# Kernel tuning notes

Hardware: AMD Instinct MI355X
Metric: run time of the kernel (lower is better)

## Reference

```python
import jax, jax.numpy as jnp
import numpy as np
from functools import partial

VOCAB = 32000
N_LAYER = 2
D_MODEL = 1024
D_INNER = 2048   # expand * d_model
D_STATE = 16
D_CONV = 4
DT_RANK = 64     # ceil(d_model/16)
SEQ_LEN = 2048   # == D_INNER (required by the repo's conv quirk)
BATCH = 1
EPS = 1e-6


def rmsnorm(x, scale):
    return x * jax.lax.rsqrt(jnp.mean(x * x, axis=-1, keepdims=True) + EPS) * scale


def setup_inputs() -> dict:
    key = jax.random.key(0)
    ks = jax.random.split(key, 16)
    s = 0.02
    L = N_LAYER
    inp = {
        "input_ids": jax.random.randint(ks[0], (BATCH, SEQ_LEN), 0, VOCAB, dtype=jnp.int32),
        "embed": jax.random.normal(ks[1], (VOCAB, D_MODEL), jnp.float32) * s,
        "norm_scale": jnp.ones((L, D_MODEL), jnp.float32),
        "in_proj_w": jax.random.normal(ks[2], (L, D_MODEL, 2 * D_INNER), jnp.float32) * s,
        "in_proj_b": jnp.zeros((L, 2 * D_INNER), jnp.float32),
        "conv_w": jax.random.normal(ks[3], (L, D_CONV, 1, SEQ_LEN), jnp.float32) * s,
        "conv_b": jnp.zeros((L, SEQ_LEN), jnp.float32),
        "x_proj_w": jax.random.normal(ks[4], (L, D_MODEL, DT_RANK + 2 * D_STATE), jnp.float32) * s,
        "dt_proj_w": jax.random.normal(ks[5], (L, DT_RANK, D_INNER), jnp.float32) * s,
        "dt_proj_b": jnp.zeros((L, D_INNER), jnp.float32),
        "out_proj_w": jax.random.normal(ks[6], (L, D_INNER, D_MODEL), jnp.float32) * s,
        "out_proj_b": jnp.zeros((L, D_MODEL), jnp.float32),
        "A_log": jnp.tile(jnp.log(jnp.arange(1, D_STATE + 1, dtype=jnp.float32)), (L, D_INNER, 1)),
        "D_param": jnp.ones((L, D_INNER), jnp.float32),
        "norm_f_scale": jnp.ones((D_MODEL,), jnp.float32),
        "lm_head_w": jax.random.normal(ks[7], (D_MODEL, VOCAB), jnp.float32) * s,
    }
    return inp


def selective_scan(u, delta, A, B, C, D):
    # u, delta: (b,l,d)   A: (d,n)   B,C: (b,l,n)   D: (d,)
    deltaA = jnp.exp(jnp.einsum('bld,dn->bldn', delta, A))            # (b,l,d,n)
    deltaB_u = delta[..., None] * B[:, :, None, :] * u[..., None]      # (b,l,d,n)

    def step(x, inps):
        dA, dBu, c = inps            # (b,d,n),(b,d,n),(b,n)
        x = dA * x + dBu
        y = jnp.einsum('bdn,bn->bd', x, c)
        return x, y

    x0 = jnp.zeros((u.shape[0], u.shape[2], A.shape[1]), u.dtype)
    _, ys = jax.lax.scan(step, x0, (jnp.moveaxis(deltaA, 1, 0),
                                    jnp.moveaxis(deltaB_u, 1, 0),
                                    jnp.moveaxis(C, 1, 0)))
    return jnp.moveaxis(ys, 0, 1) + u * D                              # (b,l,d)


def depthwise_conv(x, w, b):
    # Faithful to repo: Conv(features=SEQ_LEN, groups=D_INNER) on (b, d_inner, l).
    # With SEQ_LEN == D_INNER this is a depthwise conv over the d_inner axis.
    # x: (b, d_inner, l) as (N, W, C);  w: (d_conv, 1, SEQ_LEN)
    y = jax.lax.conv_general_dilated(x, w, window_strides=(1,), padding='SAME',
                                     dimension_numbers=('NWC', 'WIO', 'NWC'),
                                     feature_group_count=SEQ_LEN)
    return y + b


def mamba_block(h, norm_scale, in_w, in_b, conv_w, conv_b, x_proj_w,
                dt_w, dt_b, out_w, out_b, A_log, Dp):
    u = rmsnorm(h, norm_scale)
    A = -jnp.exp(A_log)
    x_and_res = u @ in_w + in_b
    x, res = jnp.split(x_and_res, 2, axis=-1)
    xt = jnp.transpose(x, (0, 2, 1))                 # (b, d_inner, l)
    xt = depthwise_conv(xt, conv_w, conv_b)[:, :, :u.shape[1]]
    x = jax.nn.silu(jnp.transpose(xt, (0, 2, 1)))     # (b, l, d_inner)
    x_dbl = u @ x_proj_w
    delta, B, C = jnp.split(x_dbl, [DT_RANK, DT_RANK + D_STATE], axis=-1)
    delta = jax.nn.softplus(delta @ dt_w + dt_b)
    y = selective_scan(x, delta, A, B, C, Dp)
    y = y * jax.nn.silu(res)
    return y @ out_w + out_b + h


def reference(input_ids, embed, norm_scale, in_proj_w, in_proj_b, conv_w, conv_b,
              x_proj_w, dt_proj_w, dt_proj_b, out_proj_w, out_proj_b, A_log,
              D_param, norm_f_scale, lm_head_w):
    h = embed[input_ids]                              # (b,l,d_model)
    for i in range(N_LAYER):
        h = mamba_block(h, norm_scale[i], in_proj_w[i], in_proj_b[i], conv_w[i],
                        conv_b[i], x_proj_w[i], dt_proj_w[i], dt_proj_b[i],
                        out_proj_w[i], out_proj_b[i], A_log[i], D_param[i])
    h = rmsnorm(h, norm_f_scale)
    return h @ lm_head_w                              # (b,l,vocab)
```

## Files before the change

### kernel.cpp

```cpp
#include <hip/hip_runtime.h>
#include <hip/hip_bf16.h>

#define SEQ 2048
#define DM  1024
#define DI  2048
#define DST 16
#define DTR 64
#define NVOC 32000
#define NVOCP 32768
#define NC  64
#define LC  32

typedef __bf16 bf16x8 __attribute__((ext_vector_type(8)));
typedef float  f32x4  __attribute__((ext_vector_type(4)));

__device__ __forceinline__ float siluf(float x) { return x / (1.f + expf(-x)); }
__device__ __forceinline__ float softplusf(float x) {
    return fmaxf(x, 0.f) + log1pf(expf(-fabsf(x)));
}
__device__ __forceinline__ unsigned short f2bf(float f) {
    union { __hip_bfloat16 h; unsigned short u; } c;
    c.h = __float2bfloat16(f);
    return c.u;
}

__global__ void embed_gather(const int* __restrict__ ids, const float* __restrict__ embed,
                             float* __restrict__ h) {
    int l = blockIdx.x;
    int row = ids[l];
    const float4* src = (const float4*)(embed + (size_t)row * DM);
    float4* dst = (float4*)(h + (size_t)l * DM);
    dst[threadIdx.x] = src[threadIdx.x];
}

__global__ void rmsnorm_kernel(const float* __restrict__ x, const float* __restrict__ w,
                               float* __restrict__ o, unsigned short* __restrict__ ob) {
    int l = blockIdx.x;
    int t = threadIdx.x;
    float4 v = ((const float4*)(x + (size_t)l * DM))[t];
    float ss = v.x*v.x + v.y*v.y + v.z*v.z + v.w*v.w;
    #pragma unroll
    for (int m = 32; m; m >>= 1) ss += __shfl_xor(ss, m);
    __shared__ float red[4];
    if ((t & 63) == 0) red[t >> 6] = ss;
    __syncthreads();
    float tot = red[0] + red[1] + red[2] + red[3];
    float sc = rsqrtf(tot * (1.f / DM) + 1e-6f);
    float4 wv = ((const float4*)w)[t];
    float4 ov;
    ov.x = v.x * sc * wv.x;
    ov.y = v.y * sc * wv.y;
    ov.z = v.z * sc * wv.z;
    ov.w = v.w * sc * wv.w;
    if (ob) {
        uint2 pk;
        pk.x = (unsigned)f2bf(ov.x) | ((unsigned)f2bf(ov.y) << 16);
        pk.y = (unsigned)f2bf(ov.z) | ((unsigned)f2bf(ov.w) << 16);
        ((uint2*)(ob + (size_t)l * DM))[t] = pk;
    } else {
        ((float4*)(o + (size_t)l * DM))[t] = ov;
    }
}

__global__ void transpose_all(const float* __restrict__ in_w, const float* __restrict__ xp_w,
                              const float* __restrict__ out_w, const float* __restrict__ dt_w,
                              const float* __restrict__ lm_w,
                              unsigned short* __restrict__ in_wT, unsigned short* __restrict__ out_wT,
                              unsigned short* __restrict__ dt_wT, unsigned short* __restrict__ lm_wT) {
    int b = blockIdx.x;
    const float* W; unsigned short* WT; int K, N, Np, loc;
    if      (b < 1024)  { W = in_w;                        WT = in_wT;                                             K=1024; N=4096;  Np=4096;  loc = b; }
    else if (b < 1056)  { W = xp_w;                        WT = in_wT + (size_t)4096 * 1024;                       K=1024; N=96;    Np=128;   loc = b - 1024; }
    else if (b < 2080)  { W = in_w + (size_t)1024 * 4096;  WT = in_wT + (size_t)4224 * 1024;                       K=1024; N=4096;  Np=4096;  loc = b - 1056; }
    else if (b < 2112)  { W = xp_w + (size_t)1024 * 96;    WT = in_wT + (size_t)4224 * 1024 + (size_t)4096 * 1024; K=1024; N=96;    Np=128;   loc = b - 2080; }
    else if (b < 2624)  { W = out_w;                       WT = out_wT;                                            K=2048; N=1024;  Np=1024;  loc = b - 2112; }
    else if (b < 3136)  { W = out_w + (size_t)2048 * 1024; WT = out_wT + (size_t)1024 * 2048;                      K=2048; N=1024;  Np=1024;  loc = b - 2624; }
    else if (b < 3168)  { W = dt_w;                        WT = dt_wT;                                             K=64;   N=2048;  Np=2048;  loc = b - 3136; }
    else if (b < 3200)  { W = dt_w + (size_t)64 * 2048;    WT = dt_wT + (size_t)2048 * 64;                         K=64;   N=2048;  Np=2048;  loc = b - 3168; }
    else                { if (!lm_wT) return; W = lm_w;    WT = lm_wT;                                             K=1024; N=32000; Np=32768; loc = b - 3200; }
    int tiles_x = Np >> 6;
    int n0 = (loc % tiles_x) * 64, k0 = (loc / tiles_x) * 64;
    __shared__ float tile[64][65];
    int tx = threadIdx.x;
    int ty = threadIdx.y;
    #pragma unroll
    for (int i = 0; i < 8; i++) {
        int r = ty + i * 8;
        int n1 = n0 + tx, n2 = n0 + tx + 32;
        tile[tx][r]      = (n1 < N) ? W[(size_t)(k0 + r) * N + n1] : 0.f;
        tile[tx + 32][r] = (n2 < N) ? W[(size_t)(k0 + r) * N + n2] : 0.f;
    }
    __syncthreads();
    int t = ty * 32 + tx;
    int nrow = t >> 5;
    int u = t & 31;
    #pragma unroll
    for (int pass = 0; pass < 8; pass++) {
        int n = pass * 8 + nrow;
        unsigned v = (unsigned)f2bf(tile[n][2 * u]) | ((unsigned)f2bf(tile[n][2 * u + 1]) << 16);
        *(unsigned*)&WT[(size_t)(n0 + n) * K + k0 + 2 * u] = v;
    }
}

template<int ACT>
__global__ __launch_bounds__(256) void gemm_f32(const float* __restrict__ A, int lda,
                                                const float* __restrict__ B,
                                                const float* __restrict__ bias,
                                                const float* __restrict__ add,
                                                float* __restrict__ C,
                                                int M, int N, int K) {
    __shared__ float As[16][68];
    __shared__ float Bs[16][64];
    int tx = threadIdx.x, ty = threadIdx.y;
    int t = ty * 16 + tx;
    int m0 = blockIdx.y * 64, n0 = blockIdx.x * 64;
    float acc[4][4] = {};
    for (int k0 = 0; k0 < K; k0 += 16) {
        #pragma unroll
        for (int i = 0; i < 4; i++) {
            int idx = t + i * 256;
            int mm = idx >> 4, kk = idx & 15;
            As[kk][mm] = A[(size_t)(m0 + mm) * lda + k0 + kk];
            int nn = idx & 63, k2 = idx >> 6;
            Bs[k2][nn] = B[(size_t)(k0 + k2) * N + n0 + nn];
        }
        __syncthreads();
        #pragma unroll
        for (int kk = 0; kk < 16; kk++) {
            float4 a = *(const float4*)&As[kk][ty * 4];
            float4 b = *(const float4*)&Bs[kk][tx * 4];
            acc[0][0] += a.x*b.x; acc[0][1] += a.x*b.y; acc[0][2] += a.x*b.z; acc[0][3] += a.x*b.w;
            acc[1][0] += a.y*b.x; acc[1][1] += a.y*b.y; acc[1][2] += a.y*b.z; acc[1][3] += a.y*b.w;
            acc[2][0] += a.z*b.x; acc[2][1] += a.z*b.y; acc[2][2] += a.z*b.z; acc[2][3] += a.z*b.w;
            acc[3][0] += a.w*b.x; acc[3][1] += a.w*b.y; acc[3][2] += a.w*b.z; acc[3][3] += a.w*b.w;
        }
        __syncthreads();
    }
    #pragma unroll
    for (int i = 0; i < 4; i++) {
        int row = m0 + ty * 4 + i;
        float4 r;
        float* pr = &r.x;
        #pragma unroll
        for (int j = 0; j < 4; j++) {
            int col = n0 + tx * 4 + j;
            float v = acc[i][j];
            if (bias) v += bias[col];
            if (add)  v += add[(size_t)row * N + col];
            if (ACT == 1) v = softplusf(v);
            pr[j] = v;
        }
        *(float4*)&C[(size_t)row * N + n0 + tx * 4] = r;
    }
}

template<int BIAS, int ADD, int ACT, int XP>
__global__ __launch_bounds__(256) void gemm_bf16(const unsigned short* __restrict__ A, int lda,
                                                 const unsigned short* __restrict__ BT,
                                                 const float* __restrict__ bias,
                                                 const float* __restrict__ add,
                                                 float* __restrict__ C,
                                                 float* __restrict__ xp_out,
                                                 unsigned short* __restrict__ aux,
                                                 int M, int N, int K) {
    __shared__ unsigned short As[128 * 32];
    __shared__ unsigned short Bs[128 * 32];
    int t = threadIdx.x;
    int w = t >> 6, l = t & 63;
    int wm = w >> 1, wn = w & 1;
    int m0 = blockIdx.x * 128;
    int n0 = blockIdx.y * 128;
    int lr = l & 15, lk = (l >> 4) * 8;
    int sr = t >> 2, sc = (t & 3) * 8;
    f32x4 acc[4][4] = {};
    for (int k0 = 0; k0 < K; k0 += 32) {
        const unsigned short* ga = A  + (size_t)(m0 + sr) * lda + k0 + sc;
        const unsigned short* gb = BT + (size_t)(n0 + sr) * K + k0 + sc;
        unsigned short* la = As + w * 512;
        unsigned short* lb = Bs + w * 512;
        __builtin_amdgcn_global_load_lds((const __attribute__((address_space(1))) void*)ga,
            (__attribute__((address_space(3))) void*)la, 16, 0, 0);
        __builtin_amdgcn_global_load_lds((const __attribute__((address_space(1))) void*)(ga + (size_t)64 * lda),
            (__attribute__((address_space(3))) void*)(la + 2048), 16, 0, 0);
        __builtin_amdgcn_global_load_lds((const __attribute__((address_space(1))) void*)gb,
            (__attribute__((address_space(3))) void*)(lb), 16, 0, 0);
        __builtin_amdgcn_global_load_lds((const __attribute__((address_space(1))) void*)(gb + (size_t)64 * K),
            (__attribute__((address_space(3))) void*)(lb + 2048), 16, 0, 0);
        __syncthreads();
        bf16x8 af[4], bfr[4];
        #pragma unroll
        for (int i = 0; i < 4; i++) {
            af[i]  = *reinterpret_cast<const bf16x8*>(&As[(wm * 64 + i * 16 + lr) * 32 + lk]);
            bfr[i] = *reinterpret_cast<const bf16x8*>(&Bs[(wn * 64 + i * 16 + lr) * 32 + lk]);
        }
        #pragma unroll
        for (int i = 0; i < 4; i++)
            #pragma unroll
            for (int j = 0; j < 4; j++)
                acc[i][j] = __builtin_amdgcn_mfma_f32_16x16x32_bf16(af[i], bfr[j], acc[i][j], 0, 0, 0);
        __syncthreads();
    }
    int cr = (l >> 4) * 4;
    if (XP && n0 >= 4096) {
        #pragma unroll
        for (int i = 0; i < 4; i++) {
            #pragma unroll
            for (int j = 0; j < 4; j++) {
                int c2 = (n0 - 4096) + wn * 64 + j * 16 + lr;
                #pragma unroll
                for (int rr = 0; rr < 4; rr++) {
                    int row = m0 + wm * 64 + i * 16 + cr + rr;
                    float v = acc[i][j][rr];
                    xp_out[(size_t)row * 128 + c2] = v;
                    if (c2 < 64) aux[(size_t)row * 64 + c2] = f2bf(v);
                }
            }
        }
    } else {
        int ldc = XP ? 4096 : N;
        #pragma unroll
        for (int i = 0; i < 4; i++) {
            #pragma unroll
            for (int j = 0; j < 4; j++) {
                int col = n0 + wn * 64 + j * 16 + lr;
                float bv = BIAS ? bias[col] : 0.f;
                #pragma unroll
                for (int rr = 0; rr < 4; rr++) {
                    int row = m0 + wm * 64 + i * 16 + cr + rr;
                    float v = acc[i][j][rr] + bv;
                    if (ADD) v += add[(size_t)row * ldc + col];
                    if (ACT == 1) v = softplusf(v);
                    C[(size_t)row * ldc + col] = v;
                }
            }
        }
    }
}

__global__ __launch_bounds__(1024, 4) void gemm_lm(
        const unsigned short* __restrict__ A,
        const unsigned short* __restrict__ BT,
        float* __restrict__ C, int M, int N, int K) {
    extern __shared__ unsigned short lds[];
    const int t = threadIdx.x;
    const int w = t >> 6, l = t & 63;
    const int wr = w >> 2, wc = w & 3;
    int bxx = blockIdx.x, byy = blockIdx.y;
    if (gridDim.x == 8 && (gridDim.y & 7) == 0) {
        int lin = blockIdx.y * 8 + blockIdx.x;
        int xcd = lin & 7, i = lin >> 3;
        bxx = i & 7;
        byy = xcd * (gridDim.y >> 3) + (i >> 3);
    }
    const int m0 = bxx * 256, n0 = byy * 256;
    const int lr = l & 15;
    const int rowA = wr * 64 + lr;
    const int rowB = wc * 64 + lr;
    const int colR = (((l >> 4) ^ (lr & 3)) * 8);
    const int srow = t >> 2;
    const int scol = (((t & 3) ^ (srow & 3)) * 8);
    const int NT = K >> 5;
    f32x4 acc[4][4] = {};
    bf16x8 af[4], bf[4];

    const unsigned short* gA = A  + (size_t)(m0 + srow) * K + scol;
    const unsigned short* gB = BT + (size_t)(n0 + srow) * K + scol;

    #pragma unroll
    for (int pp = 0; pp < 2; pp++) {
        if (pp < NT) {
            unsigned short* Ld = lds + pp * 16384;
            __builtin_amdgcn_global_load_lds(
                (const __attribute__((address_space(1))) void*)(gA + pp * 32),
                (__attribute__((address_space(3))) void*)(Ld + w * 512), 16, 0, 0);
            __builtin_amdgcn_global_load_lds(
                (const __attribute__((address_space(1))) void*)(gB + pp * 32),
                (__attribute__((address_space(3))) void*)(Ld + 8192 + w * 512), 16, 0, 0);
        }
    }

    for (int kt = 0; kt < NT; kt++) {
        if (kt >= NT - 2) { asm volatile("s_waitcnt vmcnt(0)" ::: "memory"); }
        else              { asm volatile("s_waitcnt vmcnt(2)" ::: "memory"); }
        __builtin_amdgcn_sched_barrier(0);
        __builtin_amdgcn_s_barrier();
        __builtin_amdgcn_sched_barrier(0);
        const unsigned short* Ab = lds + (kt % 3) * 16384;
        const unsigned short* Bb = Ab + 8192;
        #pragma unroll
        for (int i = 0; i < 4; i++)
            af[i] = *reinterpret_cast<const bf16x8*>(&Ab[(rowA + i * 16) * 32 + colR]);
        #pragma unroll
        for (int j = 0; j < 4; j++)
            bf[j] = *reinterpret_cast<const bf16x8*>(&Bb[(rowB + j * 16) * 32 + colR]);
        if (kt + 2 < NT) {
            unsigned short* Ld = lds + ((kt + 2) % 3) * 16384;
            __builtin_amdgcn_global_load_lds(
                (const __attribute__((address_space(1))) void*)(gA + (kt + 2) * 32),
                (__attribute__((address_space(3))) void*)(Ld + w * 512), 16, 0, 0);
            __builtin_amdgcn_global_load_lds(
                (const __attribute__((address_space(1))) void*)(gB + (kt + 2) * 32),
                (__attribute__((address_space(3))) void*)(Ld + 8192 + w * 512), 16, 0, 0);
        }
        __builtin_amdgcn_s_setprio(1);
        #pragma unroll
        for (int i = 0; i < 4; i++)
            #pragma unroll
            for (int j = 0; j < 4; j++)
                acc[i][j] = __builtin_amdgcn_mfma_f32_16x16x32_bf16(af[i], bf[j], acc[i][j], 0, 0, 0);
        __builtin_amdgcn_s_setprio(0);
    }

    float* cf = (float*)lds;
    const int cr = (l >> 4) * 4;
    for (int r = 0; r < 4; r++) {
        __syncthreads();
        if (wr == r) {
            #pragma unroll
            for (int i = 0; i < 4; i++)
                #pragma unroll
                for (int j = 0; j < 4; j++) {
                    int col = wc * 64 + j * 16 + lr;
                    #pragma unroll
                    for (int rr = 0; rr < 4; rr++)
                        cf[(i * 16 + cr + rr) * 260 + col] = acc[i][j][rr];
                }
        }
        __syncthreads();
        #pragma unroll
        for (int pass = 0; pass < 4; pass++) {
            int row = pass * 16 + (t >> 6);
            int f4 = t & 63;
            f32x4 v = *(const f32x4*)&cf[row * 260 + f4 * 4];
            int grow = m0 + r * 64 + row;
            int gcol = n0 + f4 * 4;
            if (gcol < N)
                __builtin_nontemporal_store(v, (f32x4*)&C[(size_t)grow * N + gcol]);
        }
    }
}

__global__ void xproj_kernel(const float* __restrict__ u, const float* __restrict__ xw,
                             float* __restrict__ xdbl) {
    int l0 = blockIdx.x * 4;
    int t = threadIdx.x;
    __shared__ float us[4][DM];
    for (int i = t; i < 4 * DM; i += 128) us[i >> 10][i & 1023] = u[(size_t)l0 * DM + i];
    __syncthreads();
    if (t < 96) {
        float a0 = 0.f, a1 = 0.f, a2 = 0.f, a3 = 0.f;
        for (int k = 0; k < DM; k++) {
            float wv = xw[(size_t)k * 96 + t];
            a0 += us[0][k] * wv; a1 += us[1][k] * wv;
            a2 += us[2][k] * wv; a3 += us[3][k] * wv;
        }
        xdbl[(size_t)(l0 + 0) * 128 + t] = a0;
        xdbl[(size_t)(l0 + 1) * 128 + t] = a1;
        xdbl[(size_t)(l0 + 2) * 128 + t] = a2;
        xdbl[(size_t)(l0 + 3) * 128 + t] = a3;
    }
}

__global__ __launch_bounds__(256) void scan_p1(const float* __restrict__ xr,
        const float* __restrict__ delta, const float* __restrict__ xdbl,
        const float* __restrict__ cw, const float* __restrict__ cb,
        const float* __restrict__ A_log, float* __restrict__ P, float* __restrict__ S) {
    int c = blockIdx.x;
    int d = blockIdx.y * 256 + threadIdx.x;
    int l0 = c * LC;
    __shared__ float Bsh[LC][16];
    __shared__ float cwsh[4][LC];
    __shared__ float cbsh[LC];
    {
        int t = threadIdx.x;
        #pragma unroll
        for (int i = t; i < LC * 16; i += 256) {
            int ll = i >> 4, q = i & 15;
            Bsh[ll][q] = xdbl[(size_t)(l0 + ll) * 128 + 64 + q];
        }
        if (t < LC) {
            cbsh[t] = cb[l0 + t];
            #pragma unroll
            for (int k = 0; k < 4; k++) cwsh[k][t] = cw[k * SEQ + l0 + t];
        }
    }
    __syncthreads();
    float a[16];
    #pragma unroll
    for (int i = 0; i < 4; i++) {
        float4 al = ((const float4*)(A_log + (size_t)d * 16))[i];
        a[4*i+0] = -expf(al.x); a[4*i+1] = -expf(al.y);
        a[4*i+2] = -expf(al.z); a[4*i+3] = -expf(al.w);
    }
    float s[16] = {};
    float sumdv = 0.f;
    for (int ll = 0; ll < LC; ll++) {
        size_t lrow = (size_t)(l0 + ll);
        float dv = delta[lrow * DI + d];
        const float* xrow = xr + lrow * 4096;
        float accv = cbsh[ll];
        #pragma unroll
        for (int k = 0; k < 4; k++) {
            int cc = d + k - 1;
            if (cc >= 0 && cc < DI) accv += xrow[cc] * cwsh[k][ll];
        }
        float xv = siluf(accv);
        float du = dv * xv;
        sumdv += dv;
        #pragma unroll
        for (int n = 0; n < 16; n++)
            s[n] = expf(dv * a[n]) * s[n] + du * Bsh[ll][n];
    }
    size_t o = ((size_t)c * DI + d) * 16;
    #pragma unroll
    for (int i = 0; i < 4; i++) {
        float4 sv = make_float4(s[4*i], s[4*i+1], s[4*i+2], s[4*i+3]);
        float4 pv = make_float4(expf(a[4*i]*sumdv), expf(a[4*i+1]*sumdv),
                                expf(a[4*i+2]*sumdv), expf(a[4*i+3]*sumdv));
        ((float4*)(S + o))[i] = sv;
        ((float4*)(P + o))[i] = pv;
    }
}

__global__ void scan_p2(const float* __restrict__ P, const float* __restrict__ S,
                        float* __restrict__ X) {
    int t = blockIdx.x * 256 + threadIdx.x;
    float x = 0.f;
    #pragma unroll 16
    for (int c = 0; c < NC; c++) {
        X[(size_t)c * (DI*16) + t] = x;
        x = P[(size_t)c * (DI*16) + t] * x + S[(size_t)c * (DI*16) + t];
    }
}

__global__ __launch_bounds__(256) void scan_p3(const float* __restrict__ xr,
        const float* __restrict__ delta, const float* __restrict__ xdbl,
        const float* __restrict__ cw, const float* __restrict__ cb,
        const float* __restrict__ A_log, const float* __restrict__ Dp,
        const float* __restrict__ X,
        float* __restrict__ y, unsigned short* __restrict__ yb) {
    int c = blockIdx.x;
    int d = blockIdx.y * 256 + threadIdx.x;
    int l0 = c * LC;
    __shared__ float Bsh[LC][16], Csh[LC][16];
    __shared__ float cwsh[4][LC];
    __shared__ float cbsh[LC];
    {
        int t = threadIdx.x;
        #pragma unroll
        for (int i = t; i < LC * 16; i += 256) {
            int ll = i >> 4, q = i & 15;
            size_t row = (size_t)(l0 + ll) * 128;
            Bsh[ll][q] = xdbl[row + 64 + q];
            Csh[ll][q] = xdbl[row + 80 + q];
        }
        if (t < LC) {
            cbsh[t] = cb[l0 + t];
            #pragma unroll
            for (int k = 0; k < 4; k++) cwsh[k][t] = cw[k * SEQ + l0 + t];
        }
    }
    __syncthreads();
    float a[16];
    #pragma unroll
    for (int i = 0; i < 4; i++) {
        float4 al = ((const float4*)(A_log + (size_t)d * 16))[i];
        a[4*i+0] = -expf(al.x); a[4*i+1] = -expf(al.y);
        a[4*i+2] = -expf(al.z); a[4*i+3] = -expf(al.w);
    }
    float s[16];
    size_t o = ((size_t)c * DI + d) * 16;
    #pragma unroll
    for (int i = 0; i < 4; i++) {
        float4 xv4 = ((const float4*)(X + o))[i];
        s[4*i] = xv4.x; s[4*i+1] = xv4.y; s[4*i+2] = xv4.z; s[4*i+3] = xv4.w;
    }
    float Dv = Dp[d];
    for (int ll = 0; ll < LC; ll++) {
        size_t lrow = (size_t)(l0 + ll);
        float dv = delta[lrow * DI + d];
        const float* xrow = xr + lrow * 4096;
        float accv = cbsh[ll];
        #pragma unroll
        for (int k = 0; k < 4; k++) {
            int cc = d + k - 1;
            if (cc >= 0 && cc < DI) accv += xrow[cc] * cwsh[k][ll];
        }
        float xv = siluf(accv);
        float du = dv * xv;
        float yv = 0.f;
        #pragma unroll
        for (int n = 0; n < 16; n++) {
            s[n] = expf(dv * a[n]) * s[n] + du * Bsh[ll][n];
            yv += s[n] * Csh[ll][n];
        }
        float res = xrow[2048 + d];
        float val = (yv + xv * Dv) * siluf(res);
        if (yb) yb[lrow * DI + d] = f2bf(val);
        else    y[lrow * DI + d] = val;
    }
}

extern "C" void kernel_launch(void* const* d_in, const int* in_sizes, int n_in,
                              void* d_out, int out_size, void* d_ws, size_t ws_size,
                              hipStream_t stream) {
    const int*   ids        = (const int*)d_in[0];
    const float* embed      = (const float*)d_in[1];
    const float* norm_scale = (const float*)d_in[2];
    const float* in_w       = (const float*)d_in[3];
    const float* in_b       = (const float*)d_in[4];
    const float* conv_w     = (const float*)d_in[5];
    const float* conv_b     = (const float*)d_in[6];
    const float* x_proj_w   = (const float*)d_in[7];
    const float* dt_w       = (const float*)d_in[8];
    const float* dt_b       = (const float*)d_in[9];
    const float* out_w      = (const float*)d_in[10];
    const float* out_b      = (const float*)d_in[11];
    const float* A_log      = (const float*)d_in[12];
    const float* Dp         = (const float*)d_in[13];
    const float* norm_f     = (const float*)d_in[14];
    const float* lm_w       = (const float*)d_in[15];

    float* out = (float*)d_out;

    char* p = (char*)d_ws;
    float* h  = (float*)p;  p += (size_t)SEQ * DM * 4;
    float* hn = (float*)p;  p += (size_t)SEQ * DM * 4;
    size_t base = (size_t)p - (size_t)d_ws;
    const size_t SZ_UB    = (size_t)SEQ * DM * 2;
    const size_t SZ_YB    = (size_t)SEQ * DI * 2;
    const size_t SZ_HNB   = (size_t)SEQ * DM * 2;
    const size_t SZ_DB    = (size_t)SEQ * 64 * 2;
    const size_t SZ_INWT  = (size_t)2 * 4224 * DM * 2;
    const size_t SZ_OUTWT = (size_t)2 * DM * DI * 2;
    const size_t SZ_DTWT  = (size_t)2 * DI * 64 * 2;
    const size_t SZ_LMWT  = (size_t)NVOCP * DM * 2;
    size_t need_mid  = base + SZ_UB + SZ_YB + SZ_HNB + SZ_DB + SZ_INWT + SZ_OUTWT + SZ_DTWT;
    size_t need_full = need_mid + SZ_LMWT;
    bool mid  = ws_size >= need_mid;
    bool full = ws_size >= need_full;

    unsigned short *u_b = nullptr, *y_b = nullptr, *hn_b = nullptr, *dlt_b = nullptr;
    unsigned short *in_wT = nullptr, *out_wT = nullptr, *dt_wT = nullptr, *lm_wT = nullptr;
    if (mid) {
        u_b    = (unsigned short*)p; p += SZ_UB;
        y_b    = (unsigned short*)p; p += SZ_YB;
        hn_b   = (unsigned short*)p; p += SZ_HNB;
        dlt_b  = (unsigned short*)p; p += SZ_DB;
        in_wT  = (unsigned short*)p; p += SZ_INWT;
        out_wT = (unsigned short*)p; p += SZ_OUTWT;
        dt_wT  = (unsigned short*)p; p += SZ_DTWT;
        if (full) { lm_wT = (unsigned short*)p; p += SZ_LMWT; }
    }

    float* u     = out;
    float* xr    = u + (size_t)SEQ * DM;
    float* xdbl  = xr + (size_t)SEQ * 4096;
    float* delta = xdbl + (size_t)SEQ * 128;
    float* y     = delta + (size_t)SEQ * DI;
    float* Pbuf  = y + (size_t)SEQ * DI;
    float* Sbuf  = Pbuf + (size_t)NC * DI * 16;
    float* Xbuf  = Sbuf + (size_t)NC * DI * 16;

    if (mid) {
        int nblocks = full ? 11392 : 3200;
        transpose_all<<<nblocks, dim3(32, 8), 0, stream>>>(
            in_w, x_proj_w, out_w, dt_w, lm_w, in_wT, out_wT, dt_wT, lm_wT);
    }

    embed_gather<<<SEQ, 256, 0, stream>>>(ids, embed, h);

    for (int L = 0; L < 2; L++) {
        rmsnorm_kernel<<<SEQ, 256, 0, stream>>>(h, norm_scale + (size_t)L * DM, u, u_b);
        if (mid) {
            gemm_bf16<1, 0, 0, 1><<<dim3(SEQ / 128, 4224 / 128), 256, 0, stream>>>(
                u_b, DM, in_wT + (size_t)L * 4224 * DM, in_b + (size_t)L * 4096, nullptr, xr,
                xdbl, dlt_b, SEQ, 4224, DM);
            gemm_bf16<1, 0, 1, 0><<<dim3(SEQ / 128, DI / 128), 256, 0, stream>>>(
                dlt_b, 64, dt_wT + (size_t)L * DI * 64, dt_b + (size_t)L * DI, nullptr, delta,
                nullptr, nullptr, SEQ, DI, 64);
        } else {
            gemm_f32<0><<<dim3(4096 / 64, SEQ / 64), dim3(16, 16), 0, stream>>>(
                u, DM, in_w + (size_t)L * DM * 4096, in_b + (size_t)L * 4096, nullptr, xr,
                SEQ, 4096, DM);
            xproj_kernel<<<SEQ / 4, 128, 0, stream>>>(u, x_proj_w + (size_t)L * DM * 96, xdbl);
            gemm_f32<1><<<dim3(DI / 64, SEQ / 64), dim3(16, 16), 0, stream>>>(
                xdbl, 128, dt_w + (size_t)L * DTR * DI, dt_b + (size_t)L * DI, nullptr, delta,
                SEQ, DI, DTR);
        }
        scan_p1<<<dim3(NC, DI / 256), 256, 0, stream>>>(
            xr, delta, xdbl, conv_w + (size_t)L * 4 * SEQ, conv_b + (size_t)L * SEQ,
            A_log + (size_t)L * DI * DST, Pbuf, Sbuf);
        scan_p2<<<DI * 16 / 256, 256, 0, stream>>>(Pbuf, Sbuf, Xbuf);
        scan_p3<<<dim3(NC, DI / 256), 256, 0, stream>>>(
            xr, delta, xdbl, conv_w + (size_t)L * 4 * SEQ, conv_b + (size_t)L * SEQ,
            A_log + (size_t)L * DI * DST, Dp + (size_t)L * DI, Xbuf, y, y_b);
        if (mid) {
            gemm_bf16<1, 1, 0, 0><<<dim3(SEQ / 128, DM / 128), 256, 0, stream>>>(
                y_b, DI, out_wT + (size_t)L * DM * DI, out_b + (size_t)L * DM, h, h,
                nullptr, nullptr, SEQ, DM, DI);
        } else {
            gemm_f32<0><<<dim3(DM / 64, SEQ / 64), dim3(16, 16), 0, stream>>>(
                y, DI, out_w + (size_t)L * DI * DM, out_b + (size_t)L * DM, h, h,
                SEQ, DM, DI);
        }
    }

    rmsnorm_kernel<<<SEQ, 256, 0, stream>>>(h, norm_f, hn, full ? hn_b : nullptr);
    if (full) {
        (void)hipFuncSetAttribute((const void*)gemm_lm,
                                  hipFuncAttributeMaxDynamicSharedMemorySize, 98304);
        gemm_lm<<<dim3(SEQ / 256, NVOCP / 256), 1024, 98304, stream>>>(
            hn_b, lm_wT, out, SEQ, NVOC, DM);
    } else {
        gemm_f32<0><<<dim3(NVOC / 64, SEQ / 64), dim3(16, 16), 0, stream>>>(
            hn, DM, lm_w, nullptr, nullptr, out, SEQ, NVOC, DM);
    }
}
```

Measured before the change: 773.2 us.

## Fold dt projection into in_proj GEMM via precomposed x_proj·dt weight

Precomputes the product of the delta slice of x_proj_w with dt_proj_w as an extra 2048-column bf16 weight block appended to the in_proj weight. The in_proj GEMM then emits softplus(delta) directly in its epilogue, removing the separate K=64 dt GEMM launch and its bf16 staging buffer. In exchange the main GEMM grows by 2048 columns with K=1024, which is much more arithmetic than the removed low-rank GEMM. Rounding the composed weight to bf16 also changes numerics slightly.

```diff
diff --git a/kernel.cpp b/kernel.cpp
--- a/kernel.cpp
+++ b/kernel.cpp
@@ -8,6 +8,7 @@
 #define DTR 64
 #define NVOC 32000
 #define NVOCP 32768
+#define NIN  6272
 #define NC  64
 #define LC  32
 
@@ -63,21 +64,19 @@
 }
 
 __global__ void transpose_all(const float* __restrict__ in_w, const float* __restrict__ xp_w,
-                              const float* __restrict__ out_w, const float* __restrict__ dt_w,
+                              const float* __restrict__ out_w,
                               const float* __restrict__ lm_w,
                               unsigned short* __restrict__ in_wT, unsigned short* __restrict__ out_wT,
-                              unsigned short* __restrict__ dt_wT, unsigned short* __restrict__ lm_wT) {
+                              unsigned short* __restrict__ lm_wT) {
     int b = blockIdx.x;
     const float* W; unsigned short* WT; int K, N, Np, loc;
     if      (b < 1024)  { W = in_w;                        WT = in_wT;                                             K=1024; N=4096;  Np=4096;  loc = b; }
     else if (b < 1056)  { W = xp_w;                        WT = in_wT + (size_t)4096 * 1024;                       K=1024; N=96;    Np=128;   loc = b - 1024; }
-    else if (b < 2080)  { W = in_w + (size_t)1024 * 4096;  WT = in_wT + (size_t)4224 * 1024;                       K=1024; N=4096;  Np=4096;  loc = b - 1056; }
-    else if (b < 2112)  { W = xp_w + (size_t)1024 * 96;    WT = in_wT + (size_t)4224 * 1024 + (size_t)4096 * 1024; K=1024; N=96;    Np=128;   loc = b - 2080; }
+    else if (b < 2080)  { W = in_w + (size_t)1024 * 4096;  WT = in_wT + (size_t)NIN * 1024;                        K=1024; N=4096;  Np=4096;  loc = b - 1056; }
+    else if (b < 2112)  { W = xp_w + (size_t)1024 * 96;    WT = in_wT + (size_t)NIN * 1024 + (size_t)4096 * 1024;  K=1024; N=96;    Np=128;   loc = b - 2080; }
     else if (b < 2624)  { W = out_w;                       WT = out_wT;                                            K=2048; N=1024;  Np=1024;  loc = b - 2112; }
     else if (b < 3136)  { W = out_w + (size_t)2048 * 1024; WT = out_wT + (size_t)1024 * 2048;                      K=2048; N=1024;  Np=1024;  loc = b - 2624; }
-    else if (b < 3168)  { W = dt_w;                        WT = dt_wT;                                             K=64;   N=2048;  Np=2048;  loc = b - 3136; }
-    else if (b < 3200)  { W = dt_w + (size_t)64 * 2048;    WT = dt_wT + (size_t)2048 * 64;                         K=64;   N=2048;  Np=2048;  loc = b - 3168; }
-    else                { if (!lm_wT) return; W = lm_w;    WT = lm_wT;                                             K=1024; N=32000; Np=32768; loc = b - 3200; }
+    else                { if (!lm_wT) return; W = lm_w;    WT = lm_wT;                                             K=1024; N=32000; Np=32768; loc = b - 3136; }
     int tiles_x = Np >> 6;
     int n0 = (loc % tiles_x) * 64, k0 = (loc / tiles_x) * 64;
     __shared__ float tile[64][65];
@@ -100,6 +99,35 @@
         unsigned v = (unsigned)f2bf(tile[n][2 * u]) | ((unsigned)f2bf(tile[n][2 * u + 1]) << 16);
         *(unsigned*)&WT[(size_t)(n0 + n) * K + k0 + 2 * u] = v;
     }
+}
+
+__global__ __launch_bounds__(256) void compose_dtw(const float* __restrict__ xp_w,
+                                                   const float* __restrict__ dt_w,
+                                                   unsigned short* __restrict__ in_wT) {
+    int n0 = blockIdx.x * 64, k0 = blockIdx.y * 64, L = blockIdx.z;
+    const float* xp = xp_w + (size_t)L * DM * 96;
+    const float* dw = dt_w + (size_t)L * DTR * DI;
+    unsigned short* WT = in_wT + (size_t)L * NIN * 1024 + (size_t)4224 * 1024;
+    __shared__ float xps[64][65];
+    __shared__ float dts[64][65];
+    int t = threadIdx.x;
+    for (int i = t; i < 64 * 64; i += 256) {
+        int row = i >> 6, col = i & 63;
+        xps[row][col] = xp[(size_t)(k0 + row) * 96 + col];
+        dts[row][col] = dw[(size_t)row * DI + n0 + col];
+    }
+    __syncthreads();
+    int n = t & 63, kg = t >> 6;
+    float acc[16] = {};
+    for (int r = 0; r < 64; r++) {
+        float d = dts[r][n];
+        #pragma unroll
+        for (int k = 0; k < 16; k++)
+            acc[k] += xps[kg * 16 + k][r] * d;
+    }
+    #pragma unroll
+    for (int k = 0; k < 16; k++)
+        WT[(size_t)(n0 + n) * 1024 + k0 + kg * 16 + k] = f2bf(acc[k]);
 }
 
 template<int ACT>
@@ -161,7 +189,8 @@
                                                  const float* __restrict__ add,
                                                  float* __restrict__ C,
                                                  float* __restrict__ xp_out,
-                                                 unsigned short* __restrict__ aux,
+                                                 float* __restrict__ dout,
+                                                 const float* __restrict__ dt_bias,
                                                  int M, int N, int K) {
     __shared__ unsigned short As[128 * 32];
     __shared__ unsigned short Bs[128 * 32];
@@ -201,7 +230,21 @@
         __syncthreads();
     }
     int cr = (l >> 4) * 4;
-    if (XP && n0 >= 4096) {
+    if (XP && n0 >= 4224) {
+        #pragma unroll
+        for (int i = 0; i < 4; i++) {
+            #pragma unroll
+            for (int j = 0; j < 4; j++) {
+                int c2 = (n0 - 4224) + wn * 64 + j * 16 + lr;
+                float bv = dt_bias[c2];
+                #pragma unroll
+                for (int rr = 0; rr < 4; rr++) {
+                    int row = m0 + wm * 64 + i * 16 + cr + rr;
+                    dout[(size_t)row * DI + c2] = softplusf(acc[i][j][rr] + bv);
+                }
+            }
+        }
+    } else if (XP && n0 >= 4096) {
         #pragma unroll
         for (int i = 0; i < 4; i++) {
             #pragma unroll
@@ -210,9 +253,7 @@
                 #pragma unroll
                 for (int rr = 0; rr < 4; rr++) {
                     int row = m0 + wm * 64 + i * 16 + cr + rr;
-                    float v = acc[i][j][rr];
-                    xp_out[(size_t)row * 128 + c2] = v;
-                    if (c2 < 64) aux[(size_t)row * 64 + c2] = f2bf(v);
+                    xp_out[(size_t)row * 128 + c2] = acc[i][j][rr];
                 }
             }
         }
@@ -530,26 +571,22 @@
     const size_t SZ_UB    = (size_t)SEQ * DM * 2;
     const size_t SZ_YB    = (size_t)SEQ * DI * 2;
     const size_t SZ_HNB   = (size_t)SEQ * DM * 2;
-    const size_t SZ_DB    = (size_t)SEQ * 64 * 2;
-    const size_t SZ_INWT  = (size_t)2 * 4224 * DM * 2;
+    const size_t SZ_INWT  = (size_t)2 * NIN * DM * 2;
     const size_t SZ_OUTWT = (size_t)2 * DM * DI * 2;
-    const size_t SZ_DTWT  = (size_t)2 * DI * 64 * 2;
     const size_t SZ_LMWT  = (size_t)NVOCP * DM * 2;
-    size_t need_mid  = base + SZ_UB + SZ_YB + SZ_HNB + SZ_DB + SZ_INWT + SZ_OUTWT + SZ_DTWT;
+    size_t need_mid  = base + SZ_UB + SZ_YB + SZ_HNB + SZ_INWT + SZ_OUTWT;
     size_t need_full = need_mid + SZ_LMWT;
     bool mid  = ws_size >= need_mid;
     bool full = ws_size >= need_full;
 
-    unsigned short *u_b = nullptr, *y_b = nullptr, *hn_b = nullptr, *dlt_b = nullptr;
-    unsigned short *in_wT = nullptr, *out_wT = nullptr, *dt_wT = nullptr, *lm_wT = nullptr;
+    unsigned short *u_b = nullptr, *y_b = nullptr, *hn_b = nullptr;
+    unsigned short *in_wT = nullptr, *out_wT = nullptr, *lm_wT = nullptr;
     if (mid) {
         u_b    = (unsigned short*)p; p += SZ_UB;
         y_b    = (unsigned short*)p; p += SZ_YB;
         hn_b   = (unsigned short*)p; p += SZ_HNB;
-        dlt_b  = (unsigned short*)p; p += SZ_DB;
         in_wT  = (unsigned short*)p; p += SZ_INWT;
         out_wT = (unsigned short*)p; p += SZ_OUTWT;
-        dt_wT  = (unsigned short*)p; p += SZ_DTWT;
         if (full) { lm_wT = (unsigned short*)p; p += SZ_LMWT; }
     }
 
@@ -563,9 +600,11 @@
     float* Xbuf  = Sbuf + (size_t)NC * DI * 16;
 
     if (mid) {
-        int nblocks = full ? 11392 : 3200;
+        int nblocks = full ? 11328 : 3136;
         transpose_all<<<nblocks, dim3(32, 8), 0, stream>>>(
-            in_w, x_proj_w, out_w, dt_w, lm_w, in_wT, out_wT, dt_wT, lm_wT);
+            in_w, x_proj_w, out_w, lm_w, in_wT, out_wT, lm_wT);
+        compose_dtw<<<dim3(DI / 64, DM / 64, 2), 256, 0, stream>>>(
+            x_proj_w, dt_w, in_wT);
     }
 
     embed_gather<<<SEQ, 256, 0, stream>>>(ids, embed, h);
@@ -573,12 +612,9 @@
     for (int L = 0; L < 2; L++) {
         rmsnorm_kernel<<<SEQ, 256, 0, stream>>>(h, norm_scale + (size_t)L * DM, u, u_b);
         if (mid) {
-            gemm_bf16<1, 0, 0, 1><<<dim3(SEQ / 128, 4224 / 128), 256, 0, stream>>>(
-                u_b, DM, in_wT + (size_t)L * 4224 * DM, in_b + (size_t)L * 4096, nullptr, xr,
-                xdbl, dlt_b, SEQ, 4224, DM);
-            gemm_bf16<1, 0, 1, 0><<<dim3(SEQ / 128, DI / 128), 256, 0, stream>>>(
-                dlt_b, 64, dt_wT + (size_t)L * DI * 64, dt_b + (size_t)L * DI, nullptr, delta,
-                nullptr, nullptr, SEQ, DI, 64);
+            gemm_bf16<1, 0, 0, 1><<<dim3(SEQ / 128, NIN / 128), 256, 0, stream>>>(
+                u_b, DM, in_wT + (size_t)L * NIN * DM, in_b + (size_t)L * 4096, nullptr, xr,
+                xdbl, delta, dt_b + (size_t)L * DI, SEQ, NIN, DM);
         } else {
             gemm_f32<0><<<dim3(4096 / 64, SEQ / 64), dim3(16, 16), 0, stream>>>(
                 u, DM, in_w + (size_t)L * DM * 4096, in_b + (size_t)L * 4096, nullptr, xr,
@@ -598,7 +634,7 @@
         if (mid) {
             gemm_bf16<1, 1, 0, 0><<<dim3(SEQ / 128, DM / 128), 256, 0, stream>>>(
                 y_b, DI, out_wT + (size_t)L * DM * DI, out_b + (size_t)L * DM, h, h,
-                nullptr, nullptr, SEQ, DM, DI);
+                nullptr, nullptr, nullptr, SEQ, DM, DI);
         } else {
             gemm_f32<0><<<dim3(DM / 64, SEQ / 64), dim3(16, 16), 0, stream>>>(
                 y, DI, out_w + (size_t)L * DI * DM, out_b + (size_t)L * DM, h, h,
```

New measurement: 772.7 us. No clear change (-0.1%).
